# Performance work log

Hardware: AMD Instinct MI355X
Metric: run time of the kernel (lower is better)

## Reference

```python
import jax, jax.numpy as jnp
import numpy as np

HIDDEN = 2048
NUM_HEADS = 16
HEAD_DIM = 128
FF_DIM = 8192
EPS = 1e-5


def _ln(x):
    # LayerNorm over last dim, no affine (matches nn.LayerNorm(head_dim, elementwise_affine=False))
    mu = jnp.mean(x, axis=-1, keepdims=True)
    var = jnp.mean(jnp.square(x - mu), axis=-1, keepdims=True)
    return (x - mu) * jax.lax.rsqrt(var + EPS)


def setup_inputs() -> dict:
    key = jax.random.key(0)
    ks = jax.random.split(key, 16)
    B, S, H, F = 2, 2048, HIDDEN, FF_DIM
    s = 0.02
    return {
        "hidden_states": jax.random.normal(ks[0], (B, S, H), jnp.float32),
        "temb": jax.random.normal(ks[1], (B, H), jnp.float32),
        "Wq": jax.random.normal(ks[2], (H, H), jnp.float32) * s,
        "bq": jnp.zeros((H,), jnp.float32),
        "Wk": jax.random.normal(ks[3], (H, H), jnp.float32) * s,
        "bk": jnp.zeros((H,), jnp.float32),
        "Wv": jax.random.normal(ks[4], (H, H), jnp.float32) * s,
        "bv": jnp.zeros((H,), jnp.float32),
        "Wo": jax.random.normal(ks[5], (H, H), jnp.float32) * s,
        "bo": jnp.zeros((H,), jnp.float32),
        "Wff": jax.random.normal(ks[6], (2 * F, H), jnp.float32) * s,
        "bff": jnp.zeros((2 * F,), jnp.float32),
        "Wfo": jax.random.normal(ks[7], (H, F), jnp.float32) * s,
        "bfo": jnp.zeros((H,), jnp.float32),
        "sst": jax.random.normal(ks[8], (6, H), jnp.float32) * 0.02,  # scale_shift_table
    }


def reference(hidden_states, temb, Wq, bq, Wk, bk, Wv, bv, Wo, bo, Wff, bff, Wfo, bfo, sst):
    B, S, H = hidden_states.shape
    nh, hd = NUM_HEADS, HEAD_DIM

    # adaLN modulation params: (1,6,H) + (B,1,H) -> (B,6,H)
    mods = sst[None, :, :] + temb[:, None, :]
    shift_msa, scale_msa, gate_msa, shift_mlp, scale_mlp, gate_mlp = (
        mods[:, i:i + 1, :] for i in range(6))  # each (B,1,H)

    norm_hidden = hidden_states * (1.0 + scale_msa) + shift_msa

    q = jnp.einsum('bsh,oh->bso', norm_hidden, Wq) + bq
    k = jnp.einsum('bsh,oh->bso', norm_hidden, Wk) + bk
    v = jnp.einsum('bsh,oh->bso', norm_hidden, Wv) + bv

    q = _ln(q.reshape(B, S, nh, hd))
    k = _ln(k.reshape(B, S, nh, hd))
    v = v.reshape(B, S, nh, hd)

    scale = 1.0 / (hd ** 0.5)
    # explicit attention: (B, nh, S, S)
    attn = jnp.einsum('bqnd,bknd->bnqk', q, k) * scale
    attn = jax.nn.softmax(attn, axis=-1)
    attn_out = jnp.einsum('bnqk,bknd->bqnd', attn, v).reshape(B, S, H)
    attn_out = jnp.einsum('bsh,oh->bso', attn_out, Wo) + bo

    hidden_states = hidden_states + gate_msa * attn_out

    norm_hidden = hidden_states * (1.0 + scale_mlp) + shift_mlp
    ff = jnp.einsum('bsh,oh->bso', norm_hidden, Wff) + bff
    ff, gate = ff[..., :FF_DIM], ff[..., FF_DIM:]
    ff = ff * jax.nn.gelu(gate, approximate=True)  # GEGLU, tanh gelu
    ff = jnp.einsum('bsf,of->bso', ff, Wfo) + bfo

    return hidden_states + gate_mlp * ff
```

## Files before the change

### kernel.cpp

```cpp
#include <hip/hip_runtime.h>
#include <stdint.h>

#define DEVI __device__ __forceinline__

typedef float f32x4 __attribute__((ext_vector_type(4)));
typedef __bf16 bf16x8 __attribute__((ext_vector_type(8)));

DEVI ushort f2b(float f) {
  uint32_t x = __float_as_uint(f);
  uint32_t r = (x + 0x7fffu + ((x >> 16) & 1u)) >> 16;
  return (ushort)r;
}
DEVI float b2f(ushort u) { return __uint_as_float(((uint32_t)u) << 16); }

DEVI void async_cp16(const void* g, void* l) {
  __builtin_amdgcn_global_load_lds(
      (__attribute__((address_space(1))) void*)(uintptr_t)(g),
      (__attribute__((address_space(3))) void*)(uintptr_t)(l), 16, 0, 0);
}

DEVI f32x4 MF(bf16x8 a, bf16x8 b, f32x4 c) {
  return __builtin_amdgcn_mfma_f32_16x16x32_bf16(a, b, c, 0, 0, 0);
}

#define MFENCE asm volatile("" ::: "memory")
#define BARRIER                       \
  do {                                \
    MFENCE;                           \
    __builtin_amdgcn_s_barrier();     \
    MFENCE;                           \
  } while (0)


__global__ void f32_to_bf16(const float* __restrict__ s, ushort* __restrict__ d, int n4) {
  int stride = gridDim.x * blockDim.x;
  for (int i = blockIdx.x * blockDim.x + threadIdx.x; i < n4; i += stride) {
    float4 v = ((const float4*)s)[i];
    ushort4 o;
    o.x = f2b(v.x); o.y = f2b(v.y); o.z = f2b(v.z); o.w = f2b(v.w);
    ((ushort4*)d)[i] = o;
  }
}

__global__ void mods_k(const float* __restrict__ sst, const float* __restrict__ temb,
                       float* __restrict__ mods) {
  int i = blockIdx.x * blockDim.x + threadIdx.x;
  int b = i / 12288;
  int rem = i - b * 12288;
  mods[i] = sst[rem] + temb[b * 2048 + (rem & 2047)];
}

__global__ void norm1_k(const float* __restrict__ hid, const float* __restrict__ mods,
                        ushort* __restrict__ out) {
  int i = blockIdx.x * blockDim.x + threadIdx.x;
  int e = i * 4;
  int b = e >> 22;
  int h = e & 2047;
  float4 v = ((const float4*)hid)[i];
  const float* mb = mods + b * 12288;
  float4 sc = *(const float4*)(mb + 2048 + h);
  float4 sh = *(const float4*)(mb + h);
  ushort4 o;
  o.x = f2b(v.x * (1.f + sc.x) + sh.x);
  o.y = f2b(v.y * (1.f + sc.y) + sh.y);
  o.z = f2b(v.z * (1.f + sc.z) + sh.z);
  o.w = f2b(v.w * (1.f + sc.w) + sh.w);
  ((ushort4*)out)[i] = o;
}

__global__ __launch_bounds__(256) void qk_ln(ushort* __restrict__ qkv) {
  const int rid = blockIdx.x * 4 + (threadIdx.x >> 6);
  const int L = threadIdx.x & 63;
  const int half = rid >> 16;
  const int r2 = rid & 65535;
  const int bs = r2 >> 4, head = r2 & 15;
  ushort* p = qkv + (size_t)bs * 4096 + half * 2048 + head * 128 + L * 2;
  uint32_t u = *(const uint32_t*)p;
  float e0 = b2f((ushort)(u & 0xffff));
  float e1 = b2f((ushort)(u >> 16));
  float s = e0 + e1;
#pragma unroll
  for (int d = 1; d < 64; d <<= 1) s += __shfl_xor(s, d);
  float mu = s * (1.0f / 128.0f);
  float d0 = e0 - mu, d1 = e1 - mu;
  float vq = d0 * d0 + d1 * d1;
#pragma unroll
  for (int d = 1; d < 64; d <<= 1) vq += __shfl_xor(vq, d);
  float rstd = rsqrtf(vq * (1.0f / 128.0f) + 1e-5f);
  uint32_t ou = (uint32_t)f2b(d0 * rstd) | ((uint32_t)f2b(d1 * rstd) << 16);
  *(uint32_t*)p = ou;
}


enum { EPI_QKV = 0, EPI_ATTNOUT = 1, EPI_GELU = 2, EPI_MULG = 3, EPI_FINAL = 4, EPI_VT = 5 };

template <int EPI>
__global__ __launch_bounds__(256) void gemm_bt(
    const ushort* __restrict__ A, int lda,
    const ushort* __restrict__ W, int ldw,
    const float* __restrict__ bias, int K,
    float* __restrict__ OF,
    ushort* __restrict__ OB, int ldob, int col0,
    const float* __restrict__ R0,
    const float* __restrict__ mods,
    const ushort* __restrict__ G) {
  __shared__ alignas(16) ushort As[128 * 64];
  __shared__ alignas(16) ushort Bs[128 * 64];
  const int tid = threadIdx.x;
  const int w = tid >> 6, L = tid & 63;
  const int r16 = L & 15, quad = L >> 4;
  const int m0 = blockIdx.y * 128, n0 = blockIdx.x * 128;

  f32x4 acc[4][4] = {};

  const ushort* Ag[4];
  const ushort* Bg[4];
  ushort* Al[4];
  ushort* Bl[4];
#pragma unroll
  for (int i = 0; i < 4; i++) {
    const int f = w * 4 + i, g = f >> 1, kf = f & 1;
    Ag[i] = A + (size_t)(m0 + g * 16 + r16) * lda + kf * 32 + quad * 8;
    Bg[i] = W + (size_t)(n0 + g * 16 + r16) * ldw + kf * 32 + quad * 8;
    Al[i] = &As[f * 512];
    Bl[i] = &Bs[f * 512];
  }

  const int abase = (w & 1) * 4096 + L * 8;
  const int bbase = (w >> 1) * 4096 + L * 8;

  for (int it = 0; it < K; it += 64) {
    __syncthreads();
#pragma unroll
    for (int i = 0; i < 4; i++) {
      async_cp16(Ag[i], Al[i]);
      async_cp16(Bg[i], Bl[i]);
      Ag[i] += 64;
      Bg[i] += 64;
    }
    __syncthreads();
#pragma unroll
    for (int kk = 0; kk < 2; kk++) {
      bf16x8 af[4], bfq[4];
#pragma unroll
      for (int i = 0; i < 4; i++) af[i] = *(const bf16x8*)&As[abase + (i * 2 + kk) * 512];
#pragma unroll
      for (int j = 0; j < 4; j++) bfq[j] = *(const bf16x8*)&Bs[bbase + (j * 2 + kk) * 512];
#pragma unroll
      for (int i = 0; i < 4; i++)
#pragma unroll
        for (int j = 0; j < 4; j++)
          acc[i][j] =
              __builtin_amdgcn_mfma_f32_16x16x32_bf16(af[i], bfq[j], acc[i][j], 0, 0, 0);
    }
  }

  const int wm = (w & 1) * 64, wn = (w >> 1) * 64;
#pragma unroll
  for (int ni = 0; ni < 4; ni++) {
    const int col = n0 + wn + ni * 16 + r16;
    const float bvc = bias[(EPI == EPI_VT) ? 0 : col];
#pragma unroll
    for (int mi = 0; mi < 4; mi++) {
#pragma unroll
      for (int r = 0; r < 4; r++) {
        const int row = m0 + wm + mi * 16 + quad * 4 + r;
        float v = acc[mi][ni][r] + ((EPI == EPI_VT) ? bias[row] : bvc);
        if (EPI == EPI_QKV) {
          OB[(size_t)row * ldob + col0 + col] = f2b(v);
        } else if (EPI == EPI_VT) {
          OB[(size_t)row * ldob + col] = f2b(v);
        } else if (EPI == EPI_ATTNOUT) {
          const int b = row >> 11;
          const float* mb = mods + b * 12288;
          float o = R0[(size_t)row * 2048 + col] + mb[2 * 2048 + col] * v;
          OF[(size_t)row * 2048 + col] = o;
          OB[(size_t)row * 2048 + col] =
              f2b(o * (1.0f + mb[4 * 2048 + col]) + mb[3 * 2048 + col]);
        } else if (EPI == EPI_GELU) {
          float x = v;
          float y = 0.7978845608028654f * (x + 0.044715f * x * x * x);
          float e = exp2f(-2.8853900817779268f * y);
          OB[(size_t)row * ldob + col] = f2b(x * __builtin_amdgcn_rcpf(1.0f + e));
        } else if (EPI == EPI_MULG) {
          float g = b2f(G[(size_t)row * ldob + col]);
          OB[(size_t)row * ldob + col] = f2b(v * g);
        } else {
          const int b = row >> 11;
          const float* mb = mods + b * 12288;
          size_t idx = (size_t)row * 2048 + col;
          OF[idx] = OF[idx] + mb[5 * 2048 + col] * v;
        }
      }
    }
  }
}


template <int EPI>
__global__ __launch_bounds__(512, 2) void gemm256(
    const ushort* __restrict__ A, int lda,
    const ushort* __restrict__ W, int ldw,
    const float* __restrict__ bias, int K,
    ushort* __restrict__ OB, int ldob,
    const ushort* __restrict__ G) {
  __shared__ alignas(16) ushort lds[65536];
  const int tid = threadIdx.x;
  const int w = tid >> 6, L = tid & 63;
  const int r16 = L & 15, quad = L >> 4;
  const int wm = w >> 2, wn = w & 3;
  const int m0 = blockIdx.y * 256, n0 = blockIdx.x * 256;

  const int sA = quad ^ ((r16 >> 1) & 3);
  const int kswz = 8 * ((L & 3) ^ ((L >> 3) & 3));

  const int aoff = wm * 8192 + r16 * 32 + 8 * sA;
  const int boff = 16384 + (wn >> 1) * 8192 + (wn & 1) * 2048 + r16 * 32 + 8 * sA;

  const ushort* src[8];
  int ldst[8];
#pragma unroll
  for (int i = 0; i < 8; i++) {
    const int mat = (i >> 1) & 1, kk = i >> 2;
    const int j = w * 2 + (i & 1), half = j >> 3, rg = j & 7;
    const int grow = half * 128 + rg * 16 + (L >> 2);
    src[i] = (mat ? W + (size_t)(n0 + grow) * ldw : A + (size_t)(m0 + grow) * lda) +
             kk * 32 + kswz;
    ldst[i] = mat * 16384 + half * 8192 + kk * 4096 + rg * 512;
  }

  f32x4 acc[8][4] = {};
  const int NT = K >> 6;

#pragma unroll
  for (int i = 0; i < 8; i++) {
    async_cp16(src[i], &lds[ldst[i]]);
    src[i] += 64;
  }
  asm volatile("s_waitcnt vmcnt(0)" ::: "memory");
  __builtin_amdgcn_s_barrier();
  MFENCE;

  for (int t = 0; t < NT - 1; ++t) {
    const int cb = (t & 1) << 15, nb = cb ^ 32768;
    const ushort* Ab = &lds[cb + aoff];
    const ushort* Bb = &lds[cb + boff];
    bf16x8 af[8], bq[2];

#pragma unroll
    for (int mi = 0; mi < 8; mi++) af[mi] = *(const bf16x8*)(Ab + mi * 512);
    bq[0] = *(const bf16x8*)(Bb);
    bq[1] = *(const bf16x8*)(Bb + 512);
    async_cp16(src[0], &lds[nb + ldst[0]]); src[0] += 64;
    async_cp16(src[1], &lds[nb + ldst[1]]); src[1] += 64;
    BARRIER;
    __builtin_amdgcn_s_setprio(1);
#pragma unroll
    for (int mi = 0; mi < 8; mi++) {
      acc[mi][0] = MF(af[mi], bq[0], acc[mi][0]);
      acc[mi][1] = MF(af[mi], bq[1], acc[mi][1]);
    }
    __builtin_amdgcn_s_setprio(0);
    BARRIER;

    bq[0] = *(const bf16x8*)(Bb + 1024);
    bq[1] = *(const bf16x8*)(Bb + 1536);
    async_cp16(src[2], &lds[nb + ldst[2]]); src[2] += 64;
    async_cp16(src[3], &lds[nb + ldst[3]]); src[3] += 64;
    BARRIER;
    __builtin_amdgcn_s_setprio(1);
#pragma unroll
    for (int mi = 0; mi < 8; mi++) {
      acc[mi][2] = MF(af[mi], bq[0], acc[mi][2]);
      acc[mi][3] = MF(af[mi], bq[1], acc[mi][3]);
    }
    __builtin_amdgcn_s_setprio(0);
    asm volatile("s_waitcnt vmcnt(4)" ::: "memory");
    __builtin_amdgcn_s_barrier();
    MFENCE;

#pragma unroll
    for (int mi = 0; mi < 8; mi++) af[mi] = *(const bf16x8*)(Ab + 4096 + mi * 512);
    bq[0] = *(const bf16x8*)(Bb + 4096);
    bq[1] = *(const bf16x8*)(Bb + 4096 + 512);
    async_cp16(src[4], &lds[nb + ldst[4]]); src[4] += 64;
    async_cp16(src[5], &lds[nb + ldst[5]]); src[5] += 64;
    BARRIER;
    __builtin_amdgcn_s_setprio(1);
#pragma unroll
    for (int mi = 0; mi < 8; mi++) {
      acc[mi][0] = MF(af[mi], bq[0], acc[mi][0]);
      acc[mi][1] = MF(af[mi], bq[1], acc[mi][1]);
    }
    __builtin_amdgcn_s_setprio(0);
    BARRIER;

    bq[0] = *(const bf16x8*)(Bb + 4096 + 1024);
    bq[1] = *(const bf16x8*)(Bb + 4096 + 1536);
    async_cp16(src[6], &lds[nb + ldst[6]]); src[6] += 64;
    async_cp16(src[7], &lds[nb + ldst[7]]); src[7] += 64;
    BARRIER;
    __builtin_amdgcn_s_setprio(1);
#pragma unroll
    for (int mi = 0; mi < 8; mi++) {
      acc[mi][2] = MF(af[mi], bq[0], acc[mi][2]);
      acc[mi][3] = MF(af[mi], bq[1], acc[mi][3]);
    }
    __builtin_amdgcn_s_setprio(0);
    asm volatile("s_waitcnt vmcnt(4)" ::: "memory");
    __builtin_amdgcn_s_barrier();
    MFENCE;
  }

  {
    const int cb = ((NT - 1) & 1) << 15;
    const ushort* Ab = &lds[cb + aoff];
    const ushort* Bb = &lds[cb + boff];
    bf16x8 af[8], bq[4];
#pragma unroll
    for (int mi = 0; mi < 8; mi++) af[mi] = *(const bf16x8*)(Ab + mi * 512);
#pragma unroll
    for (int ni = 0; ni < 4; ni++) bq[ni] = *(const bf16x8*)(Bb + ni * 512);
#pragma unroll
    for (int mi = 0; mi < 8; mi++)
#pragma unroll
      for (int ni = 0; ni < 4; ni++) acc[mi][ni] = MF(af[mi], bq[ni], acc[mi][ni]);
    asm volatile("s_waitcnt vmcnt(0)" ::: "memory");
    __builtin_amdgcn_s_barrier();
    MFENCE;
#pragma unroll
    for (int mi = 0; mi < 8; mi++) af[mi] = *(const bf16x8*)(Ab + 4096 + mi * 512);
#pragma unroll
    for (int ni = 0; ni < 4; ni++) bq[ni] = *(const bf16x8*)(Bb + 4096 + ni * 512);
#pragma unroll
    for (int mi = 0; mi < 8; mi++)
#pragma unroll
      for (int ni = 0; ni < 4; ni++) acc[mi][ni] = MF(af[mi], bq[ni], acc[mi][ni]);
  }

#pragma unroll
  for (int ni = 0; ni < 4; ni++) {
    const int col = n0 + wn * 64 + ni * 16 + r16;
    const float bvc = bias[col];
#pragma unroll
    for (int mi = 0; mi < 8; mi++) {
      const int row = m0 + wm * 128 + mi * 16 + quad * 4;
#pragma unroll
      for (int r = 0; r < 4; r++) {
        float v = acc[mi][ni][r] + bvc;
        size_t idx = (size_t)(row + r) * ldob + col;
        if (EPI == EPI_GELU) {
          float x = v;
          float y = 0.7978845608028654f * (x + 0.044715f * x * x * x);
          float e = exp2f(-2.8853900817779268f * y);
          OB[idx] = f2b(x * __builtin_amdgcn_rcpf(1.0f + e));
        } else {
          float g = b2f(G[idx]);
          OB[idx] = f2b(v * g);
        }
      }
    }
  }
}

__global__ __launch_bounds__(256) void attn_kernel(const ushort* __restrict__ qkv,
                                                   const ushort* __restrict__ vt,
                                                   ushort* __restrict__ out) {
  constexpr int S = 2048;
  __shared__ alignas(16) ushort Ks[8192];
  __shared__ alignas(16) ushort Vs[8192];
  __shared__ alignas(16) ushort Ps[4096];
  const int b = blockIdx.z, h = blockIdx.y, q0 = blockIdx.x * 64;
  const int tid = threadIdx.x, w = tid >> 6, L = tid & 63;
  const int r16 = L & 15, quad = L >> 4;

  bf16x8 aq[4];
  {
    const ushort* qb = qkv + (size_t)(b * S + q0 + w * 16 + r16) * 4096 + h * 128 + quad * 8;
#pragma unroll
    for (int kk = 0; kk < 4; kk++) aq[kk] = *(const bf16x8*)(qb + kk * 32);
  }

  const ushort* kb[4];
  const ushort* vb[4];
  ushort* kl[4];
  ushort* vl[4];
#pragma unroll
  for (int i = 0; i < 4; i++) {
    const int f = w * 4 + i;
    const int nt = f >> 2, kk = f & 3;
    kb[i] = qkv + (size_t)(b * S + nt * 16 + r16) * 4096 + 2048 + h * 128 + kk * 32 + quad * 8;
    kl[i] = &Ks[f * 512];
    const int dt = f >> 1, kk2 = f & 1;
    vb[i] = vt + (size_t)(h * 128 + dt * 16 + r16) * 4096 + b * S + kk2 * 32 + quad * 8;
    vl[i] = &Vs[f * 512];
  }

  float m_i[4] = {-1e30f, -1e30f, -1e30f, -1e30f};
  float l_i[4] = {0.f, 0.f, 0.f, 0.f};
  f32x4 o[8] = {};
  const float cl = 0.08838834764831845f * 1.4426950408889634f;

  for (int kt = 0; kt < 32; kt++) {
    const int k0 = kt * 64;
    __syncthreads();
#pragma unroll
    for (int i = 0; i < 4; i++) {
      async_cp16(kb[i] + (size_t)k0 * 4096, kl[i]);
      async_cp16(vb[i] + k0, vl[i]);
    }
    __syncthreads();

    f32x4 sf[4];
#pragma unroll
    for (int nt = 0; nt < 4; nt++) {
      f32x4 a = {};
#pragma unroll
      for (int kk = 0; kk < 4; kk++) {
        bf16x8 bk = *(const bf16x8*)&Ks[((nt * 4 + kk) * 64 + L) * 8];
        a = __builtin_amdgcn_mfma_f32_16x16x32_bf16(aq[kk], bk, a, 0, 0, 0);
      }
      sf[nt] = a;
    }

    float al[4];
    float pv[4][4];
#pragma unroll
    for (int r = 0; r < 4; r++) {
      float mx = fmaxf(fmaxf(sf[0][r], sf[1][r]), fmaxf(sf[2][r], sf[3][r]));
      mx = fmaxf(mx, __shfl_xor(mx, 1));
      mx = fmaxf(mx, __shfl_xor(mx, 2));
      mx = fmaxf(mx, __shfl_xor(mx, 4));
      mx = fmaxf(mx, __shfl_xor(mx, 8));
      float mnew = fmaxf(m_i[r], mx);
      al[r] = exp2f((m_i[r] - mnew) * cl);
      m_i[r] = mnew;
      float rs = 0.f;
#pragma unroll
      for (int nt = 0; nt < 4; nt++) {
        float p = exp2f((sf[nt][r] - mnew) * cl);
        pv[nt][r] = p;
        rs += p;
      }
      rs += __shfl_xor(rs, 1);
      rs += __shfl_xor(rs, 2);
      rs += __shfl_xor(rs, 4);
      rs += __shfl_xor(rs, 8);
      l_i[r] = l_i[r] * al[r] + rs;
    }

#pragma unroll
    for (int nt = 0; nt < 4; nt++)
#pragma unroll
      for (int r = 0; r < 4; r++) {
        const int q = quad * 4 + r;
        const int addr =
            (w * 16 + q) * 64 + (((nt * 2 + (r16 >> 3)) ^ (q & 7)) << 3) + (r16 & 7);
        Ps[addr] = f2b(pv[nt][r]);
      }

#pragma unroll
    for (int dt = 0; dt < 8; dt++) {
      f32x4 t = o[dt];
      t[0] *= al[0]; t[1] *= al[1]; t[2] *= al[2]; t[3] *= al[3];
      o[dt] = t;
    }
    __syncthreads();

    bf16x8 ap[2];
#pragma unroll
    for (int kk2 = 0; kk2 < 2; kk2++)
      ap[kk2] = *(const bf16x8*)
          &Ps[(w * 16 + r16) * 64 + (((kk2 * 4 + quad) ^ (r16 & 7)) << 3)];
#pragma unroll
    for (int dt = 0; dt < 8; dt++) {
#pragma unroll
      for (int kk2 = 0; kk2 < 2; kk2++) {
        bf16x8 bv = *(const bf16x8*)&Vs[((dt * 2 + kk2) * 64 + L) * 8];
        o[dt] = __builtin_amdgcn_mfma_f32_16x16x32_bf16(ap[kk2], bv, o[dt], 0, 0, 0);
      }
    }
  }

  float linv[4];
#pragma unroll
  for (int r = 0; r < 4; r++) linv[r] = 1.0f / l_i[r];
#pragma unroll
  for (int dt = 0; dt < 8; dt++)
#pragma unroll
    for (int r = 0; r < 4; r++) {
      int row = q0 + w * 16 + quad * 4 + r;
      out[(size_t)(b * S + row) * 2048 + h * 128 + dt * 16 + r16] = f2b(o[dt][r] * linv[r]);
    }
}


extern "C" void kernel_launch(void* const* d_in, const int* in_sizes, int n_in,
                              void* d_out, int out_size, void* d_ws, size_t ws_size,
                              hipStream_t stream) {
  const float* hidden = (const float*)d_in[0];
  const float* temb = (const float*)d_in[1];
  const float* Wq = (const float*)d_in[2];
  const float* bq = (const float*)d_in[3];
  const float* Wk = (const float*)d_in[4];
  const float* bk = (const float*)d_in[5];
  const float* Wv = (const float*)d_in[6];
  const float* bv = (const float*)d_in[7];
  const float* Wo = (const float*)d_in[8];
  const float* bo = (const float*)d_in[9];
  const float* Wff = (const float*)d_in[10];
  const float* bff = (const float*)d_in[11];
  const float* Wfo = (const float*)d_in[12];
  const float* bfo = (const float*)d_in[13];
  const float* sst = (const float*)d_in[14];
  float* out = (float*)d_out;

  char* ws = (char*)d_ws;
  size_t off = 0;
  auto alloc = [&](size_t bytes) {
    void* p = ws + off;
    off += (bytes + 255) & ~(size_t)255;
    return p;
  };
  ushort* wWq = (ushort*)alloc(4194304ull * 2);
  ushort* wWk = (ushort*)alloc(4194304ull * 2);
  ushort* wWv = (ushort*)alloc(4194304ull * 2);
  ushort* wWo = (ushort*)alloc(4194304ull * 2);
  ushort* wWff = (ushort*)alloc(33554432ull * 2);
  ushort* wWfo = (ushort*)alloc(16777216ull * 2);
  float* modsb = (float*)alloc(24576ull * 4);
  ushort* normb = (ushort*)alloc(8388608ull * 2);
  ushort* qkvb = (ushort*)alloc(4096ull * 4096 * 2);
  ushort* vtb = (ushort*)alloc(2048ull * 4096 * 2);
  ushort* attnb = (ushort*)alloc(8388608ull * 2);
  ushort* ffgb = (ushort*)alloc(33554432ull * 2);
  ushort* gb = qkvb;

  const int T = 256;
  f32_to_bf16<<<1024, T, 0, stream>>>(Wq, wWq, 1048576);
  f32_to_bf16<<<1024, T, 0, stream>>>(Wk, wWk, 1048576);
  f32_to_bf16<<<1024, T, 0, stream>>>(Wv, wWv, 1048576);
  f32_to_bf16<<<1024, T, 0, stream>>>(Wo, wWo, 1048576);
  f32_to_bf16<<<2048, T, 0, stream>>>(Wff, wWff, 8388608);
  f32_to_bf16<<<2048, T, 0, stream>>>(Wfo, wWfo, 4194304);
  mods_k<<<96, T, 0, stream>>>(sst, temb, modsb);
  norm1_k<<<8192, T, 0, stream>>>(hidden, modsb, normb);

  dim3 gq(16, 32);
  gemm_bt<EPI_QKV><<<gq, T, 0, stream>>>(normb, 2048, wWq, 2048, bq, 2048, nullptr, qkvb,
                                         4096, 0, nullptr, nullptr, nullptr);
  gemm_bt<EPI_QKV><<<gq, T, 0, stream>>>(normb, 2048, wWk, 2048, bk, 2048, nullptr, qkvb,
                                         4096, 2048, nullptr, nullptr, nullptr);
  gemm_bt<EPI_VT><<<dim3(32, 16), T, 0, stream>>>(wWv, 2048, normb, 2048, bv, 2048, nullptr,
                                                  vtb, 4096, 0, nullptr, nullptr, nullptr);
  qk_ln<<<32768, T, 0, stream>>>(qkvb);
  attn_kernel<<<dim3(32, 16, 2), T, 0, stream>>>(qkvb, vtb, attnb);
  gemm_bt<EPI_ATTNOUT><<<gq, T, 0, stream>>>(attnb, 2048, wWo, 2048, bo, 2048, out, normb,
                                             2048, 0, hidden, modsb, nullptr);
  dim3 g256(32, 16);
  gemm256<EPI_GELU><<<g256, 512, 0, stream>>>(normb, 2048, wWff + (size_t)8192 * 2048, 2048,
                                              bff + 8192, 2048, gb, 8192, nullptr);
  gemm256<EPI_MULG><<<g256, 512, 0, stream>>>(normb, 2048, wWff, 2048, bff, 2048, ffgb,
                                              8192, gb);
  gemm_bt<EPI_FINAL><<<gq, T, 0, stream>>>(ffgb, 8192, wWfo, 8192, bfo, 8192, out, nullptr,
                                           0, 0, nullptr, modsb, nullptr);
}
```

Measured before the change: 1.496 ms.

## Replace 128x128 GEMM with double-buffered 128x256 kernel and XCD-aware tile swizzle

Replaces the simple 128x128 single-buffered gemm_bt with a 512-thread 128x256 tile kernel. It double-buffers LDS with async global-to-LDS copies, uses swizzled LDS layouts, raises MFMA priority, and waits with partial vmcnt so loads overlap compute. It also remaps workgroup IDs in both GEMM kernels so that neighbouring tiles are grouped across the 8 XCDs, aiming for better L2 reuse. This gives larger tiles and fewer blocks, and the tile remap and barrier choreography are new places where correctness could break.

```diff
diff --git a/kernel.cpp b/kernel.cpp
--- a/kernel.cpp
+++ b/kernel.cpp
@@ -91,80 +91,138 @@
   *(uint32_t*)p = ou;
 }
 
-
 enum { EPI_QKV = 0, EPI_ATTNOUT = 1, EPI_GELU = 2, EPI_MULG = 3, EPI_FINAL = 4, EPI_VT = 5 };
 
+
 template <int EPI>
-__global__ __launch_bounds__(256) void gemm_bt(
+__global__ __launch_bounds__(512, 2) void gemm128(
     const ushort* __restrict__ A, int lda,
     const ushort* __restrict__ W, int ldw,
     const float* __restrict__ bias, int K,
     float* __restrict__ OF,
     ushort* __restrict__ OB, int ldob, int col0,
     const float* __restrict__ R0,
-    const float* __restrict__ mods,
-    const ushort* __restrict__ G) {
-  __shared__ alignas(16) ushort As[128 * 64];
-  __shared__ alignas(16) ushort Bs[128 * 64];
+    const float* __restrict__ mods) {
+  __shared__ alignas(16) ushort lds[49152];
   const int tid = threadIdx.x;
   const int w = tid >> 6, L = tid & 63;
   const int r16 = L & 15, quad = L >> 4;
-  const int m0 = blockIdx.y * 128, n0 = blockIdx.x * 128;
+  const int wm = w >> 2, wn = w & 3;
+
+  const int nwg = gridDim.x * gridDim.y;
+  const int id0 = blockIdx.y * gridDim.x + blockIdx.x;
+  const int swz = (id0 & 7) * (nwg >> 3) + (id0 >> 3);
+  const int m0 = (swz / gridDim.x) * 128, n0 = (swz % gridDim.x) * 256;
+
+  const int sA = quad ^ ((r16 >> 1) & 3);
+  const int kswz = 8 * ((L & 3) ^ ((L >> 3) & 3));
+
+  const int aoff = wm * 2048 + r16 * 32 + 8 * sA;
+  const int boff = 8192 + wn * 2048 + r16 * 32 + 8 * sA;
+
+  const ushort* src[6];
+  int ldst[6];
+#pragma unroll
+  for (int i = 0; i < 6; i++) {
+    const int kk = i / 3, s = i % 3;
+    const int rg = (s == 2) ? (8 + w) : w;
+    const int grow = rg * 16 + (L >> 2);
+    src[i] = (s ? W + (size_t)(n0 + grow) * ldw : A + (size_t)(m0 + grow) * lda) +
+             kk * 32 + kswz;
+    ldst[i] = s ? (8192 + kk * 8192 + rg * 512) : (kk * 4096 + w * 512);
+  }
 
   f32x4 acc[4][4] = {};
-
-  const ushort* Ag[4];
-  const ushort* Bg[4];
-  ushort* Al[4];
-  ushort* Bl[4];
-#pragma unroll
-  for (int i = 0; i < 4; i++) {
-    const int f = w * 4 + i, g = f >> 1, kf = f & 1;
-    Ag[i] = A + (size_t)(m0 + g * 16 + r16) * lda + kf * 32 + quad * 8;
-    Bg[i] = W + (size_t)(n0 + g * 16 + r16) * ldw + kf * 32 + quad * 8;
-    Al[i] = &As[f * 512];
-    Bl[i] = &Bs[f * 512];
-  }
-
-  const int abase = (w & 1) * 4096 + L * 8;
-  const int bbase = (w >> 1) * 4096 + L * 8;
-
-  for (int it = 0; it < K; it += 64) {
-    __syncthreads();
-#pragma unroll
-    for (int i = 0; i < 4; i++) {
-      async_cp16(Ag[i], Al[i]);
-      async_cp16(Bg[i], Bl[i]);
-      Ag[i] += 64;
-      Bg[i] += 64;
-    }
-    __syncthreads();
-#pragma unroll
-    for (int kk = 0; kk < 2; kk++) {
-      bf16x8 af[4], bfq[4];
-#pragma unroll
-      for (int i = 0; i < 4; i++) af[i] = *(const bf16x8*)&As[abase + (i * 2 + kk) * 512];
-#pragma unroll
-      for (int j = 0; j < 4; j++) bfq[j] = *(const bf16x8*)&Bs[bbase + (j * 2 + kk) * 512];
-#pragma unroll
-      for (int i = 0; i < 4; i++)
-#pragma unroll
-        for (int j = 0; j < 4; j++)
-          acc[i][j] =
-              __builtin_amdgcn_mfma_f32_16x16x32_bf16(af[i], bfq[j], acc[i][j], 0, 0, 0);
-    }
-  }
-
-  const int wm = (w & 1) * 64, wn = (w >> 1) * 64;
+  const int NT = K >> 6;
+
+#pragma unroll
+  for (int i = 0; i < 6; i++) {
+    async_cp16(src[i], &lds[ldst[i]]);
+    src[i] += 64;
+  }
+  asm volatile("s_waitcnt vmcnt(0)" ::: "memory");
+  __builtin_amdgcn_s_barrier();
+  MFENCE;
+
+  for (int t = 0; t < NT - 1; ++t) {
+    const int cb = (t & 1) * 24576, nb = cb ^ 24576;
+    const ushort* Ab = &lds[cb + aoff];
+    const ushort* Bb = &lds[cb + boff];
+    bf16x8 af[4], bq[4];
+
+#pragma unroll
+    for (int mi = 0; mi < 4; mi++) af[mi] = *(const bf16x8*)(Ab + mi * 512);
+#pragma unroll
+    for (int ni = 0; ni < 4; ni++) bq[ni] = *(const bf16x8*)(Bb + ni * 512);
+    async_cp16(src[0], &lds[nb + ldst[0]]); src[0] += 64;
+    async_cp16(src[1], &lds[nb + ldst[1]]); src[1] += 64;
+    async_cp16(src[2], &lds[nb + ldst[2]]); src[2] += 64;
+    BARRIER;
+    __builtin_amdgcn_s_setprio(1);
+#pragma unroll
+    for (int mi = 0; mi < 4; mi++)
+#pragma unroll
+      for (int ni = 0; ni < 4; ni++) acc[mi][ni] = MF(af[mi], bq[ni], acc[mi][ni]);
+    __builtin_amdgcn_s_setprio(0);
+    asm volatile("s_waitcnt vmcnt(3)" ::: "memory");
+    __builtin_amdgcn_s_barrier();
+    MFENCE;
+
+#pragma unroll
+    for (int mi = 0; mi < 4; mi++) af[mi] = *(const bf16x8*)(Ab + 4096 + mi * 512);
+#pragma unroll
+    for (int ni = 0; ni < 4; ni++) bq[ni] = *(const bf16x8*)(Bb + 8192 + ni * 512);
+    async_cp16(src[3], &lds[nb + ldst[3]]); src[3] += 64;
+    async_cp16(src[4], &lds[nb + ldst[4]]); src[4] += 64;
+    async_cp16(src[5], &lds[nb + ldst[5]]); src[5] += 64;
+    BARRIER;
+    __builtin_amdgcn_s_setprio(1);
+#pragma unroll
+    for (int mi = 0; mi < 4; mi++)
+#pragma unroll
+      for (int ni = 0; ni < 4; ni++) acc[mi][ni] = MF(af[mi], bq[ni], acc[mi][ni]);
+    __builtin_amdgcn_s_setprio(0);
+    asm volatile("s_waitcnt vmcnt(3)" ::: "memory");
+    __builtin_amdgcn_s_barrier();
+    MFENCE;
+  }
+
+  {
+    const int cb = ((NT - 1) & 1) * 24576;
+    const ushort* Ab = &lds[cb + aoff];
+    const ushort* Bb = &lds[cb + boff];
+    bf16x8 af[4], bq[4];
+#pragma unroll
+    for (int mi = 0; mi < 4; mi++) af[mi] = *(const bf16x8*)(Ab + mi * 512);
+#pragma unroll
+    for (int ni = 0; ni < 4; ni++) bq[ni] = *(const bf16x8*)(Bb + ni * 512);
+#pragma unroll
+    for (int mi = 0; mi < 4; mi++)
+#pragma unroll
+      for (int ni = 0; ni < 4; ni++) acc[mi][ni] = MF(af[mi], bq[ni], acc[mi][ni]);
+    asm volatile("s_waitcnt vmcnt(0)" ::: "memory");
+    __builtin_amdgcn_s_barrier();
+    MFENCE;
+#pragma unroll
+    for (int mi = 0; mi < 4; mi++) af[mi] = *(const bf16x8*)(Ab + 4096 + mi * 512);
+#pragma unroll
+    for (int ni = 0; ni < 4; ni++) bq[ni] = *(const bf16x8*)(Bb + 8192 + ni * 512);
+#pragma unroll
+    for (int mi = 0; mi < 4; mi++)
+#pragma unroll
+      for (int ni = 0; ni < 4; ni++) acc[mi][ni] = MF(af[mi], bq[ni], acc[mi][ni]);
+  }
+
 #pragma unroll
   for (int ni = 0; ni < 4; ni++) {
-    const int col = n0 + wn + ni * 16 + r16;
+    const int col = n0 + wn * 64 + ni * 16 + r16;
     const float bvc = bias[(EPI == EPI_VT) ? 0 : col];
 #pragma unroll
     for (int mi = 0; mi < 4; mi++) {
+      const int row0 = m0 + wm * 64 + mi * 16 + quad * 4;
 #pragma unroll
       for (int r = 0; r < 4; r++) {
-        const int row = m0 + wm + mi * 16 + quad * 4 + r;
+        const int row = row0 + r;
         float v = acc[mi][ni][r] + ((EPI == EPI_VT) ? bias[row] : bvc);
         if (EPI == EPI_QKV) {
           OB[(size_t)row * ldob + col0 + col] = f2b(v);
@@ -177,14 +235,6 @@
           OF[(size_t)row * 2048 + col] = o;
           OB[(size_t)row * 2048 + col] =
               f2b(o * (1.0f + mb[4 * 2048 + col]) + mb[3 * 2048 + col]);
-        } else if (EPI == EPI_GELU) {
-          float x = v;
-          float y = 0.7978845608028654f * (x + 0.044715f * x * x * x);
-          float e = exp2f(-2.8853900817779268f * y);
-          OB[(size_t)row * ldob + col] = f2b(x * __builtin_amdgcn_rcpf(1.0f + e));
-        } else if (EPI == EPI_MULG) {
-          float g = b2f(G[(size_t)row * ldob + col]);
-          OB[(size_t)row * ldob + col] = f2b(v * g);
         } else {
           const int b = row >> 11;
           const float* mb = mods + b * 12288;
@@ -209,7 +259,11 @@
   const int w = tid >> 6, L = tid & 63;
   const int r16 = L & 15, quad = L >> 4;
   const int wm = w >> 2, wn = w & 3;
-  const int m0 = blockIdx.y * 256, n0 = blockIdx.x * 256;
+
+  const int nwg = gridDim.x * gridDim.y;
+  const int id0 = blockIdx.y * gridDim.x + blockIdx.x;
+  const int swz = (id0 & 7) * (nwg >> 3) + (id0 >> 3);
+  const int m0 = (swz / gridDim.x) * 256, n0 = (swz % gridDim.x) * 256;
 
   const int sA = quad ^ ((r16 >> 1) & 3);
   const int kswz = 8 * ((L & 3) ^ ((L >> 3) & 3));
@@ -546,22 +600,22 @@
   mods_k<<<96, T, 0, stream>>>(sst, temb, modsb);
   norm1_k<<<8192, T, 0, stream>>>(hidden, modsb, normb);
 
-  dim3 gq(16, 32);
-  gemm_bt<EPI_QKV><<<gq, T, 0, stream>>>(normb, 2048, wWq, 2048, bq, 2048, nullptr, qkvb,
-                                         4096, 0, nullptr, nullptr, nullptr);
-  gemm_bt<EPI_QKV><<<gq, T, 0, stream>>>(normb, 2048, wWk, 2048, bk, 2048, nullptr, qkvb,
-                                         4096, 2048, nullptr, nullptr, nullptr);
-  gemm_bt<EPI_VT><<<dim3(32, 16), T, 0, stream>>>(wWv, 2048, normb, 2048, bv, 2048, nullptr,
-                                                  vtb, 4096, 0, nullptr, nullptr, nullptr);
+  dim3 g128(8, 32);
+  gemm128<EPI_QKV><<<g128, 512, 0, stream>>>(normb, 2048, wWq, 2048, bq, 2048, nullptr,
+                                             qkvb, 4096, 0, nullptr, nullptr);
+  gemm128<EPI_QKV><<<g128, 512, 0, stream>>>(normb, 2048, wWk, 2048, bk, 2048, nullptr,
+                                             qkvb, 4096, 2048, nullptr, nullptr);
+  gemm128<EPI_VT><<<dim3(16, 16), 512, 0, stream>>>(wWv, 2048, normb, 2048, bv, 2048,
+                                                    nullptr, vtb, 4096, 0, nullptr, nullptr);
   qk_ln<<<32768, T, 0, stream>>>(qkvb);
   attn_kernel<<<dim3(32, 16, 2), T, 0, stream>>>(qkvb, vtb, attnb);
-  gemm_bt<EPI_ATTNOUT><<<gq, T, 0, stream>>>(attnb, 2048, wWo, 2048, bo, 2048, out, normb,
-                                             2048, 0, hidden, modsb, nullptr);
+  gemm128<EPI_ATTNOUT><<<g128, 512, 0, stream>>>(attnb, 2048, wWo, 2048, bo, 2048, out,
+                                                 normb, 2048, 0, hidden, modsb);
   dim3 g256(32, 16);
   gemm256<EPI_GELU><<<g256, 512, 0, stream>>>(normb, 2048, wWff + (size_t)8192 * 2048, 2048,
                                               bff + 8192, 2048, gb, 8192, nullptr);
   gemm256<EPI_MULG><<<g256, 512, 0, stream>>>(normb, 2048, wWff, 2048, bff, 2048, ffgb,
                                               8192, gb);
-  gemm_bt<EPI_FINAL><<<gq, T, 0, stream>>>(ffgb, 8192, wWfo, 8192, bfo, 8192, out, nullptr,
-                                           0, 0, nullptr, modsb, nullptr);
-}
+  gemm128<EPI_FINAL><<<g128, 512, 0, stream>>>(ffgb, 8192, wWfo, 8192, bfo, 8192, out,
+                                               nullptr, 0, 0, nullptr, modsb);
+}
```

After: 1.268 ms. 1.18x faster.
